# Optimization experiments

Hardware: AMD Instinct MI355X
Metric: run time of the kernel (lower is better)

The kernel has to match this reference:

```python
import jax, jax.numpy as jnp
import numpy as np

DIM = 1024
HEADS = 16
HEAD_DIM = DIM // HEADS
BS, SQ, SK = 4, 2048, 2048


def setup_inputs() -> dict:
    key = jax.random.key(0)
    ks = jax.random.split(key, 12)
    s = 1.0 / np.sqrt(DIM)
    return {
        "x_q": jax.random.normal(ks[0], (BS, SQ, DIM), jnp.float32),
        "x_k": jax.random.normal(ks[1], (BS, SK, DIM), jnp.float32),
        "x_v": jax.random.normal(ks[2], (BS, SK, DIM), jnp.float32),
        "mask": jax.random.randint(ks[3], (BS, SQ, SK), 0, 2, jnp.int32),
        # torch nn.Linear weights: [out, in]; y = x @ W.T + b
        "wq": jax.random.uniform(ks[4], (DIM, DIM), jnp.float32, -s, s),
        "bq": jax.random.uniform(ks[5], (DIM,), jnp.float32, -s, s),
        "wk": jax.random.uniform(ks[6], (DIM, DIM), jnp.float32, -s, s),
        "bk": jax.random.uniform(ks[7], (DIM,), jnp.float32, -s, s),
        "wv": jax.random.uniform(ks[8], (DIM, DIM), jnp.float32, -s, s),
        "bv": jax.random.uniform(ks[9], (DIM,), jnp.float32, -s, s),
        "wo": jax.random.uniform(ks[10], (DIM, DIM), jnp.float32, -s, s),
        "bo": jax.random.uniform(ks[11], (DIM,), jnp.float32, -s, s),
    }


def reference(x_q, x_k, x_v, mask, wq, bq, wk, bk, wv, bv, wo, bo):
    bs, sq, dim = x_q.shape
    q = x_q @ wq.T + bq
    k = x_k @ wk.T + bk
    v = x_v @ wv.T + bv
    # [b, h, s, d]
    qh = q.reshape(bs, sq, HEADS, HEAD_DIM).transpose(0, 2, 1, 3)
    kh = k.reshape(bs, -1, HEADS, HEAD_DIM).transpose(0, 2, 1, 3)
    vh = v.reshape(bs, -1, HEADS, HEAD_DIM).transpose(0, 2, 1, 3)
    scale = 1.0 / np.sqrt(HEAD_DIM).astype(np.float32)
    s = jnp.einsum("bhqd,bhkd->bhqk", qh, kh) * scale
    # mask==0 positions set to -10000 across all heads
    s = jnp.where(mask[:, None, :, :] == 0, jnp.float32(-10000.0), s)
    p = jax.nn.softmax(s, axis=-1)
    z = jnp.einsum("bhqk,bhkd->bhqd", p, vh)
    z = z.transpose(0, 2, 1, 3).reshape(bs, sq, dim)
    return z @ wo.T + bo
```

## Files before the change

kernel.cpp:

```cpp
#include <hip/hip_runtime.h>

#define DEVINL __device__ __forceinline__

typedef _Float16 half8 __attribute__((ext_vector_type(8)));
typedef __fp16 fp16x2 __attribute__((ext_vector_type(2)));
typedef float f32x4 __attribute__((ext_vector_type(4)));
typedef float float4v __attribute__((ext_vector_type(4)));

static constexpr int kDIM = 1024;
static constexpr int kHEADS = 16;
static constexpr int kHD = 64;
static constexpr int kBS = 4;
static constexpr int kSQ = 2048;
static constexpr int kSK = 2048;
static constexpr int kMTOT = kBS * kSQ;

DEVINL void async_copy16(void* lds, const void* g) {
  __builtin_amdgcn_global_load_lds(
      (__attribute__((address_space(1))) unsigned int*)(g),
      (__attribute__((address_space(3))) unsigned int*)(lds), 16, 0, 0);
}

DEVINL unsigned pkrtz_u32(float a, float b) {
  fp16x2 h = __builtin_amdgcn_cvt_pkrtz(a, b);
  unsigned u;
  __builtin_memcpy(&u, &h, 4);
  return u;
}

__global__ void pack_mask_kernel(const int* __restrict__ mask,
                                 unsigned* __restrict__ bits) {
  int t = blockIdx.x * blockDim.x + threadIdx.x;
  const int4* p = (const int4*)(mask + (size_t)t * 32);
  unsigned w = 0;
#pragma unroll
  for (int j = 0; j < 8; ++j) {
    int4 v = p[j];
    w |= (v.x != 0 ? 1u : 0u) << (j * 4);
    w |= (v.y != 0 ? 1u : 0u) << (j * 4 + 1);
    w |= (v.z != 0 ? 1u : 0u) << (j * 4 + 2);
    w |= (v.w != 0 ? 1u : 0u) << (j * 4 + 3);
  }
  bits[t] = w;
}

__global__ void cvt4_kernel(const float* __restrict__ s0, const float* __restrict__ s1,
                            const float* __restrict__ s2, const float* __restrict__ s3,
                            _Float16* __restrict__ d0, _Float16* __restrict__ d1,
                            _Float16* __restrict__ d2, _Float16* __restrict__ d3) {
  int which = blockIdx.x >> 9;
  const float* s = which == 0 ? s0 : which == 1 ? s1 : which == 2 ? s2 : s3;
  _Float16* d = which == 0 ? d0 : which == 1 ? d1 : which == 2 ? d2 : d3;
  int j = ((blockIdx.x & 511) * 256 + threadIdx.x) * 8;
  float4v a0 = *(const float4v*)(s + j);
  float4v a1 = *(const float4v*)(s + j + 4);
  half8 h;
  h[0] = (_Float16)a0[0]; h[1] = (_Float16)a0[1];
  h[2] = (_Float16)a0[2]; h[3] = (_Float16)a0[3];
  h[4] = (_Float16)a1[0]; h[5] = (_Float16)a1[1];
  h[6] = (_Float16)a1[2]; h[7] = (_Float16)a1[3];
  *(half8*)(d + j) = h;
}

template <bool A_F32, bool OUT_F16>
__launch_bounds__(256, 2)
__global__ void gemm_bt_kernel(const void* __restrict__ Aptr,
                               const _Float16* __restrict__ B,
                               const float* __restrict__ bias,
                               void* __restrict__ Cptr, int M, int N, int K) {
  __shared__ __align__(16) _Float16 As[128 * 64];
  __shared__ __align__(16) _Float16 Bs[128 * 64];
  const int tid = threadIdx.x;
  const int lane = tid & 63;
  const int w = tid >> 6;
  const int wr = w >> 1, wc = w & 1;
  const int bm0 = blockIdx.y * 128;
  const int bn0 = blockIdx.x * 128;
  const int c16 = lane & 15;
  const int hi4 = lane >> 4;

  f32x4 acc[4][4] = {};

  for (int k0 = 0; k0 < K; k0 += 64) {
    __syncthreads();
    if (A_F32) {
      const float* A32 = (const float*)Aptr;
#pragma unroll
      for (int i = 0; i < 4; ++i) {
        int c = i * 256 + tid;
        int row = c >> 3, seg = c & 7;
        int gseg = seg ^ (row & 7);
        const float* src = A32 + (size_t)(bm0 + row) * K + k0 + gseg * 8;
        float4v a0 = *(const float4v*)src;
        float4v a1 = *(const float4v*)(src + 4);
        half8 h;
        h[0] = (_Float16)a0[0]; h[1] = (_Float16)a0[1];
        h[2] = (_Float16)a0[2]; h[3] = (_Float16)a0[3];
        h[4] = (_Float16)a1[0]; h[5] = (_Float16)a1[1];
        h[6] = (_Float16)a1[2]; h[7] = (_Float16)a1[3];
        *(half8*)((char*)As + c * 16) = h;
      }
    } else {
      const _Float16* A16 = (const _Float16*)Aptr;
#pragma unroll
      for (int i = 0; i < 4; ++i) {
        int c = i * 256 + tid;
        int row = c >> 3, seg = c & 7;
        int gseg = seg ^ (row & 7);
        async_copy16((char*)As + i * 4096 + w * 1024,
                     A16 + (size_t)(bm0 + row) * K + k0 + gseg * 8);
      }
    }
#pragma unroll
    for (int i = 0; i < 4; ++i) {
      int c = i * 256 + tid;
      int row = c >> 3, seg = c & 7;
      int gseg = seg ^ (row & 7);
      async_copy16((char*)Bs + i * 4096 + w * 1024,
                   B + (size_t)(bn0 + row) * K + k0 + gseg * 8);
    }
    __syncthreads();
#pragma unroll
    for (int kf = 0; kf < 2; ++kf) {
      half8 af[4], bf[4];
#pragma unroll
      for (int m = 0; m < 4; ++m) {
        int row = wr * 64 + m * 16 + c16;
        int off = row * 128 + (((kf * 4 + hi4) << 4) ^ ((row & 7) << 4));
        af[m] = *(const half8*)((const char*)As + off);
      }
#pragma unroll
      for (int n = 0; n < 4; ++n) {
        int row = wc * 64 + n * 16 + c16;
        int off = row * 128 + (((kf * 4 + hi4) << 4) ^ ((row & 7) << 4));
        bf[n] = *(const half8*)((const char*)Bs + off);
      }
#pragma unroll
      for (int m = 0; m < 4; ++m)
#pragma unroll
        for (int n = 0; n < 4; ++n)
          acc[m][n] =
              __builtin_amdgcn_mfma_f32_16x16x32_f16(af[m], bf[n], acc[m][n], 0, 0, 0);
    }
  }
#pragma unroll
  for (int n = 0; n < 4; ++n) {
    int col = bn0 + wc * 64 + n * 16 + c16;
    float bv = bias[col];
#pragma unroll
    for (int m = 0; m < 4; ++m) {
      int row0 = bm0 + wr * 64 + m * 16 + (hi4 << 2);
#pragma unroll
      for (int r = 0; r < 4; ++r) {
        float v = acc[m][n][r] + bv;
        if (OUT_F16)
          ((_Float16*)Cptr)[(size_t)(row0 + r) * N + col] = (_Float16)v;
        else
          ((float*)Cptr)[(size_t)(row0 + r) * N + col] = v;
      }
    }
  }
}

__global__ void transpose_v_kernel(const _Float16* __restrict__ V,
                                   _Float16* __restrict__ Vt) {
  __shared__ _Float16 tile[64][72];
  int bh = blockIdx.y;
  int b = bh >> 4, h = bh & 15;
  int s0 = blockIdx.x * 64;
  int tid = threadIdx.x;
  {
    int s = tid >> 2, dseg = tid & 3;
    const half8* src =
        (const half8*)(V + (size_t)(b * kSK + s0 + s) * kDIM + h * 64 + dseg * 16);
    half8 v0 = src[0], v1 = src[1];
#pragma unroll
    for (int j = 0; j < 8; ++j) {
      tile[s][dseg * 16 + j] = v0[j];
      tile[s][dseg * 16 + 8 + j] = v1[j];
    }
  }
  __syncthreads();
  {
    int d = tid >> 2, sseg = tid & 3;
    half8 o0, o1;
#pragma unroll
    for (int j = 0; j < 8; ++j) {
      o0[j] = tile[sseg * 16 + j][d];
      o1[j] = tile[sseg * 16 + 8 + j][d];
    }
    half8* dst = (half8*)(Vt + ((size_t)(bh * 64 + d)) * kSK + s0 + sseg * 16);
    dst[0] = o0;
    dst[1] = o1;
  }
}

__launch_bounds__(256, 3)
__global__ void attn_kernel(const _Float16* __restrict__ Q,
                            const _Float16* __restrict__ K,
                            const _Float16* __restrict__ Vt,
                            const unsigned* __restrict__ maskbits,
                            _Float16* __restrict__ Z) {
  __shared__ __align__(16) char smem[32768 + 128 * 72 * 2];
  _Float16* Ps = (_Float16*)(smem + 32768);
  const int tid = threadIdx.x, lane = tid & 63, w = tid >> 6;
  const int b = blockIdx.z, h = blockIdx.y, qt0 = blockIdx.x * 128;
  const int c16 = lane & 15;
  const int hi4 = lane >> 4;
  const int row4 = hi4 << 2;
  const unsigned* mb = maskbits + (size_t)b * kSQ * (kSK / 32);

#pragma unroll
  for (int i = 0; i < 4; ++i) {
    int c = i * 256 + tid;
    int row = c >> 3, seg = c & 7;
    int gseg = seg ^ (row & 7);
    async_copy16(smem + i * 4096 + w * 1024,
                 Q + (size_t)(b * kSQ + qt0 + row) * kDIM + h * 64 + gseg * 8);
  }
  __syncthreads();
  half8 qf[2][2];
#pragma unroll
  for (int m = 0; m < 2; ++m)
#pragma unroll
    for (int kf = 0; kf < 2; ++kf) {
      int row = w * 32 + m * 16 + c16;
      int off = row * 128 + (((kf * 4 + hi4) << 4) ^ ((row & 7) << 4));
      qf[m][kf] = *(const half8*)(smem + off);
      qf[m][kf] *= (_Float16)0.18033688f;
    }
  __syncthreads();

  auto stage_kv = [&](int bufoff, int ktt) {
#pragma unroll
    for (int i = 0; i < 2; ++i) {
      int c = i * 256 + tid;
      int row = c >> 3, seg = c & 7;
      int gseg = seg ^ (row & 7);
      async_copy16(smem + bufoff + i * 4096 + w * 1024,
                   K + (size_t)(b * kSK + ktt + row) * kDIM + h * 64 + gseg * 8);
    }
#pragma unroll
    for (int i = 0; i < 2; ++i) {
      int c = i * 256 + tid;
      int row = c >> 3, seg = c & 7;
      int gseg = seg ^ (row & 7);
      async_copy16(smem + bufoff + 8192 + i * 4096 + w * 1024,
                   Vt + (size_t)((b * kHEADS + h) * kHD + row) * kSK + ktt + gseg * 8);
    }
  };

  unsigned long long mq_cur[2], mq_nxt[2];
  stage_kv(0, 0);
#pragma unroll
  for (int m2 = 0; m2 < 2; ++m2) {
    int q = qt0 + w * 32 + m2 * 16 + c16;
    mq_cur[m2] = *(const unsigned long long*)(mb + (size_t)q * (kSK / 32));
  }
  asm volatile("s_waitcnt vmcnt(0)" ::: "memory");
  __builtin_amdgcn_s_barrier();
  asm volatile("" ::: "memory");

  f32x4 zacc[2][4] = {};
  f32x4 lacc[2] = {};
  half8 ones8;
#pragma unroll
  for (int j = 0; j < 8; ++j) ones8[j] = (_Float16)1.0f;

  int cur = 0;
  for (int kt = 0; kt < kSK; kt += 64) {
    if (kt + 64 < kSK) {
      stage_kv((cur ^ 1) * 16384, kt + 64);
#pragma unroll
      for (int m2 = 0; m2 < 2; ++m2) {
        int q = qt0 + w * 32 + m2 * 16 + c16;
        mq_nxt[m2] = *(const unsigned long long*)(mb + (size_t)q * (kSK / 32) +
                                                  ((kt + 64) >> 5));
      }
    }
    const char* bufK = smem + cur * 16384;
    const char* bufV = bufK + 8192;

    f32x4 s[2][4] = {};
    __builtin_amdgcn_s_setprio(1);
#pragma unroll
    for (int kf = 0; kf < 2; ++kf)
#pragma unroll
      for (int n = 0; n < 4; ++n) {
        int key = n * 16 + c16;
        half8 kb = *(const half8*)(bufK + key * 128 +
                                   (((kf * 4 + hi4) << 4) ^ ((key & 7) << 4)));
        s[0][n] = __builtin_amdgcn_mfma_f32_16x16x32_f16(kb, qf[0][kf], s[0][n], 0, 0, 0);
        s[1][n] = __builtin_amdgcn_mfma_f32_16x16x32_f16(kb, qf[1][kf], s[1][n], 0, 0, 0);
      }
    __builtin_amdgcn_s_setprio(0);

#pragma unroll
    for (int m2 = 0; m2 < 2; ++m2) {
      unsigned lo = (unsigned)(mq_cur[m2] >> (hi4 * 4));
      unsigned hh = (unsigned)(mq_cur[m2] >> (hi4 * 4 + 32));
      int q_local = w * 32 + m2 * 16 + c16;
#pragma unroll
      for (int n = 0; n < 4; ++n) {
        unsigned sel = (n < 2) ? lo : hh;
        const int base = (n & 1) * 16;
        float p[4];
#pragma unroll
        for (int r = 0; r < 4; ++r) {
          float pv = __builtin_exp2f(s[m2][n][r]);
          int msk = __builtin_amdgcn_sbfe((int)sel, base + r, 1);
          pv = __uint_as_float(__float_as_uint(pv) & (unsigned)msk);
          p[r] = pv;
        }
        uint2 pw = {pkrtz_u32(p[0], p[1]), pkrtz_u32(p[2], p[3])};
        *(uint2*)((char*)Ps + q_local * 144 + n * 32 + hi4 * 8) = pw;
      }
    }

    __builtin_amdgcn_s_setprio(1);
#pragma unroll
    for (int kf2 = 0; kf2 < 2; ++kf2) {
      half8 vb[4];
#pragma unroll
      for (int df = 0; df < 4; ++df) {
        int d = df * 16 + c16;
        vb[df] = *(const half8*)(bufV + d * 128 +
                                 (((kf2 * 4 + hi4) << 4) ^ ((d & 7) << 4)));
      }
#pragma unroll
      for (int m2 = 0; m2 < 2; ++m2) {
        int q_local = w * 32 + m2 * 16 + c16;
        half8 pa = *(const half8*)((char*)Ps + q_local * 144 + (kf2 * 4 + hi4) * 16);
        lacc[m2] = __builtin_amdgcn_mfma_f32_16x16x32_f16(pa, ones8, lacc[m2], 0, 0, 0);
#pragma unroll
        for (int df = 0; df < 4; ++df)
          zacc[m2][df] =
              __builtin_amdgcn_mfma_f32_16x16x32_f16(pa, vb[df], zacc[m2][df], 0, 0, 0);
      }
    }
    __builtin_amdgcn_s_setprio(0);

    asm volatile("s_waitcnt vmcnt(0)" ::: "memory");
    __builtin_amdgcn_s_barrier();
    asm volatile("" ::: "memory");
    mq_cur[0] = mq_nxt[0];
    mq_cur[1] = mq_nxt[1];
    cur ^= 1;
  }

#pragma unroll
  for (int m2 = 0; m2 < 2; ++m2)
#pragma unroll
    for (int r = 0; r < 4; ++r) {
      float inv = 1.0f / lacc[m2][r];
      int q = qt0 + w * 32 + m2 * 16 + row4 + r;
#pragma unroll
      for (int df = 0; df < 4; ++df) {
        int d = df * 16 + c16;
        Z[(size_t)(b * kSQ + q) * kDIM + h * 64 + d] =
            (_Float16)(zacc[m2][df][r] * inv);
      }
    }
}

extern "C" void kernel_launch(void* const* d_in, const int* in_sizes, int n_in,
                              void* d_out, int out_size, void* d_ws,
                              size_t ws_size, hipStream_t stream) {
  const float* x_q = (const float*)d_in[0];
  const float* x_k = (const float*)d_in[1];
  const float* x_v = (const float*)d_in[2];
  const int* mask = (const int*)d_in[3];
  const float* wq = (const float*)d_in[4];
  const float* bq = (const float*)d_in[5];
  const float* wk = (const float*)d_in[6];
  const float* bk = (const float*)d_in[7];
  const float* wv = (const float*)d_in[8];
  const float* bv = (const float*)d_in[9];
  const float* wo = (const float*)d_in[10];
  const float* bo = (const float*)d_in[11];

  const size_t W_ELEMS = (size_t)1024 * 1024;
  const size_t T_ELEMS = (size_t)kMTOT * kDIM;
  const size_t NEED = (4 * W_ELEMS + 5 * T_ELEMS) * 2 + (size_t)kBS * kSQ * (kSK / 32) * 4;
  if (ws_size < NEED) return;

  char* ws = (char*)d_ws;
  _Float16* Wq16 = (_Float16*)ws;
  _Float16* Wk16 = Wq16 + W_ELEMS;
  _Float16* Wv16 = Wk16 + W_ELEMS;
  _Float16* Wo16 = Wv16 + W_ELEMS;
  _Float16* Q16 = Wo16 + W_ELEMS;
  _Float16* K16 = Q16 + T_ELEMS;
  _Float16* V16 = K16 + T_ELEMS;
  _Float16* Vt16 = V16 + T_ELEMS;
  _Float16* Z16 = Vt16 + T_ELEMS;
  unsigned* mbits = (unsigned*)(Z16 + T_ELEMS);

  pack_mask_kernel<<<2048, 256, 0, stream>>>(mask, mbits);
  cvt4_kernel<<<2048, 256, 0, stream>>>(wq, wk, wv, wo, Wq16, Wk16, Wv16, Wo16);

  dim3 gg(8, 64);
  gemm_bt_kernel<true, true><<<gg, 256, 0, stream>>>(x_q, Wq16, bq, Q16, kMTOT, kDIM, kDIM);
  gemm_bt_kernel<true, true><<<gg, 256, 0, stream>>>(x_k, Wk16, bk, K16, kMTOT, kDIM, kDIM);
  gemm_bt_kernel<true, true><<<gg, 256, 0, stream>>>(x_v, Wv16, bv, V16, kMTOT, kDIM, kDIM);

  transpose_v_kernel<<<dim3(32, 64), 256, 0, stream>>>(V16, Vt16);

  attn_kernel<<<dim3(16, 16, 4), 256, 0, stream>>>(Q16, K16, Vt16, mbits, Z16);

  gemm_bt_kernel<false, false><<<gg, 256, 0, stream>>>(Z16, Wo16, bo, d_out, kMTOT, kDIM, kDIM);
}
```

Baseline: 317.4 us.

## Enlarge attention block to 256 queries and interleave softmax with PV halves

The attention kernel now runs 512-thread blocks covering 256 query rows instead of 128. Each staged K/V tile is therefore shared by 8 waves, halving global and L2 traffic per query, and each thread issues only one async copy for K and one for V. The softmax/PV stage is split into two 32-key halves, so the P scratch buffer shrinks to 80-byte padded rows and exp work interleaves with MFMA. LDS offsets are also precomputed outside the loop. In exchange the grid has half as many blocks, and the new launch bounds may constrain registers and occupancy.

```diff
diff --git a/kernel.cpp b/kernel.cpp
--- a/kernel.cpp
+++ b/kernel.cpp
@@ -195,16 +195,16 @@
   }
 }
 
-__launch_bounds__(256, 3)
+__launch_bounds__(512, 4)
 __global__ void attn_kernel(const _Float16* __restrict__ Q,
                             const _Float16* __restrict__ K,
                             const _Float16* __restrict__ Vt,
                             const unsigned* __restrict__ maskbits,
                             _Float16* __restrict__ Z) {
-  __shared__ __align__(16) char smem[32768 + 128 * 72 * 2];
-  _Float16* Ps = (_Float16*)(smem + 32768);
+  __shared__ __align__(16) char smem[32768 + 256 * 80];
+  char* Ps = smem + 32768;
   const int tid = threadIdx.x, lane = tid & 63, w = tid >> 6;
-  const int b = blockIdx.z, h = blockIdx.y, qt0 = blockIdx.x * 128;
+  const int b = blockIdx.z, h = blockIdx.y, qt0 = blockIdx.x * 256;
   const int c16 = lane & 15;
   const int hi4 = lane >> 4;
   const int row4 = hi4 << 2;
@@ -212,10 +212,10 @@
 
 #pragma unroll
   for (int i = 0; i < 4; ++i) {
-    int c = i * 256 + tid;
+    int c = i * 512 + tid;
     int row = c >> 3, seg = c & 7;
     int gseg = seg ^ (row & 7);
-    async_copy16(smem + i * 4096 + w * 1024,
+    async_copy16(smem + i * 8192 + w * 1024,
                  Q + (size_t)(b * kSQ + qt0 + row) * kDIM + h * 64 + gseg * 8);
   }
   __syncthreads();
@@ -231,23 +231,36 @@
     }
   __syncthreads();
 
+  int kb_off[2][4];
+#pragma unroll
+  for (int kf = 0; kf < 2; ++kf)
+#pragma unroll
+    for (int n = 0; n < 4; ++n) {
+      int key = n * 16 + c16;
+      kb_off[kf][n] = key * 128 + (((kf * 4 + hi4) << 4) ^ ((key & 7) << 4));
+    }
+  int vb_off[2][4];
+#pragma unroll
+  for (int kfh = 0; kfh < 2; ++kfh)
+#pragma unroll
+    for (int df = 0; df < 4; ++df) {
+      int d = df * 16 + c16;
+      vb_off[kfh][df] = d * 128 + (((kfh * 4 + hi4) << 4) ^ ((d & 7) << 4));
+    }
+  int ps_w[2], ps_r[2];
+#pragma unroll
+  for (int m2 = 0; m2 < 2; ++m2) {
+    int q_local = w * 32 + m2 * 16 + c16;
+    ps_w[m2] = q_local * 80 + hi4 * 8;
+    ps_r[m2] = q_local * 80 + hi4 * 16;
+  }
+
+  const int srow = tid >> 3, sseg = (tid & 7) ^ ((tid >> 3) & 7);
   auto stage_kv = [&](int bufoff, int ktt) {
-#pragma unroll
-    for (int i = 0; i < 2; ++i) {
-      int c = i * 256 + tid;
-      int row = c >> 3, seg = c & 7;
-      int gseg = seg ^ (row & 7);
-      async_copy16(smem + bufoff + i * 4096 + w * 1024,
-                   K + (size_t)(b * kSK + ktt + row) * kDIM + h * 64 + gseg * 8);
-    }
-#pragma unroll
-    for (int i = 0; i < 2; ++i) {
-      int c = i * 256 + tid;
-      int row = c >> 3, seg = c & 7;
-      int gseg = seg ^ (row & 7);
-      async_copy16(smem + bufoff + 8192 + i * 4096 + w * 1024,
-                   Vt + (size_t)((b * kHEADS + h) * kHD + row) * kSK + ktt + gseg * 8);
-    }
+    async_copy16(smem + bufoff + w * 1024,
+                 K + (size_t)(b * kSK + ktt + srow) * kDIM + h * 64 + sseg * 8);
+    async_copy16(smem + bufoff + 8192 + w * 1024,
+                 Vt + (size_t)((b * kHEADS + h) * kHD + srow) * kSK + ktt + sseg * 8);
   };
 
   unsigned long long mq_cur[2], mq_nxt[2];
@@ -287,58 +300,49 @@
     for (int kf = 0; kf < 2; ++kf)
 #pragma unroll
       for (int n = 0; n < 4; ++n) {
-        int key = n * 16 + c16;
-        half8 kb = *(const half8*)(bufK + key * 128 +
-                                   (((kf * 4 + hi4) << 4) ^ ((key & 7) << 4)));
+        half8 kb = *(const half8*)(bufK + kb_off[kf][n]);
         s[0][n] = __builtin_amdgcn_mfma_f32_16x16x32_f16(kb, qf[0][kf], s[0][n], 0, 0, 0);
         s[1][n] = __builtin_amdgcn_mfma_f32_16x16x32_f16(kb, qf[1][kf], s[1][n], 0, 0, 0);
       }
     __builtin_amdgcn_s_setprio(0);
 
 #pragma unroll
-    for (int m2 = 0; m2 < 2; ++m2) {
-      unsigned lo = (unsigned)(mq_cur[m2] >> (hi4 * 4));
-      unsigned hh = (unsigned)(mq_cur[m2] >> (hi4 * 4 + 32));
-      int q_local = w * 32 + m2 * 16 + c16;
-#pragma unroll
-      for (int n = 0; n < 4; ++n) {
-        unsigned sel = (n < 2) ? lo : hh;
-        const int base = (n & 1) * 16;
-        float p[4];
-#pragma unroll
-        for (int r = 0; r < 4; ++r) {
-          float pv = __builtin_exp2f(s[m2][n][r]);
-          int msk = __builtin_amdgcn_sbfe((int)sel, base + r, 1);
-          pv = __uint_as_float(__float_as_uint(pv) & (unsigned)msk);
-          p[r] = pv;
+    for (int kfh = 0; kfh < 2; ++kfh) {
+#pragma unroll
+      for (int m2 = 0; m2 < 2; ++m2) {
+        unsigned selw = (kfh == 0) ? (unsigned)(mq_cur[m2] >> (hi4 * 4))
+                                   : (unsigned)(mq_cur[m2] >> (hi4 * 4 + 32));
+#pragma unroll
+        for (int nn = 0; nn < 2; ++nn) {
+          const int base = nn * 16;
+          float p[4];
+#pragma unroll
+          for (int r = 0; r < 4; ++r) {
+            float pv = __builtin_exp2f(s[m2][kfh * 2 + nn][r]);
+            int msk = __builtin_amdgcn_sbfe((int)selw, base + r, 1);
+            pv = __uint_as_float(__float_as_uint(pv) & (unsigned)msk);
+            p[r] = pv;
+          }
+          uint2 pw = {pkrtz_u32(p[0], p[1]), pkrtz_u32(p[2], p[3])};
+          *(uint2*)(Ps + ps_w[m2] + nn * 32) = pw;
         }
-        uint2 pw = {pkrtz_u32(p[0], p[1]), pkrtz_u32(p[2], p[3])};
-        *(uint2*)((char*)Ps + q_local * 144 + n * 32 + hi4 * 8) = pw;
-      }
-    }
-
-    __builtin_amdgcn_s_setprio(1);
-#pragma unroll
-    for (int kf2 = 0; kf2 < 2; ++kf2) {
+      }
+      __builtin_amdgcn_s_setprio(1);
       half8 vb[4];
 #pragma unroll
-      for (int df = 0; df < 4; ++df) {
-        int d = df * 16 + c16;
-        vb[df] = *(const half8*)(bufV + d * 128 +
-                                 (((kf2 * 4 + hi4) << 4) ^ ((d & 7) << 4)));
-      }
+      for (int df = 0; df < 4; ++df)
+        vb[df] = *(const half8*)(bufV + vb_off[kfh][df]);
 #pragma unroll
       for (int m2 = 0; m2 < 2; ++m2) {
-        int q_local = w * 32 + m2 * 16 + c16;
-        half8 pa = *(const half8*)((char*)Ps + q_local * 144 + (kf2 * 4 + hi4) * 16);
+        half8 pa = *(const half8*)(Ps + ps_r[m2]);
         lacc[m2] = __builtin_amdgcn_mfma_f32_16x16x32_f16(pa, ones8, lacc[m2], 0, 0, 0);
 #pragma unroll
         for (int df = 0; df < 4; ++df)
           zacc[m2][df] =
               __builtin_amdgcn_mfma_f32_16x16x32_f16(pa, vb[df], zacc[m2][df], 0, 0, 0);
       }
-    }
-    __builtin_amdgcn_s_setprio(0);
+      __builtin_amdgcn_s_setprio(0);
+    }
 
     asm volatile("s_waitcnt vmcnt(0)" ::: "memory");
     __builtin_amdgcn_s_barrier();
@@ -406,7 +410,7 @@
 
   transpose_v_kernel<<<dim3(32, 64), 256, 0, stream>>>(V16, Vt16);
 
-  attn_kernel<<<dim3(16, 16, 4), 256, 0, stream>>>(Q16, K16, Vt16, mbits, Z16);
+  attn_kernel<<<dim3(8, 16, 4), 512, 0, stream>>>(Q16, K16, Vt16, mbits, Z16);
 
   gemm_bt_kernel<false, false><<<gg, 256, 0, stream>>>(Z16, Wo16, bo, d_out, kMTOT, kDIM, kDIM);
 }
```

Result: slower. 328.6 us (+3.5%).
